# Kernel tuning notes

Hardware: AMD Instinct MI355X
Metric: run time of the kernel (lower is better)

The kernel has to match this reference:

```python
import jax, jax.numpy as jnp
import numpy as np

NUM_HEADS = 16
HEAD_DIM = 64
INPUT_DIM = 1024
EMBED_DIM = NUM_HEADS * HEAD_DIM  # 1024


def setup_inputs() -> dict:
    key = jax.random.key(0)
    ks = jax.random.split(key, 9)
    B, S = 4, 2048
    scale = 1.0 / np.sqrt(INPUT_DIM)
    return {
        "q": jax.random.normal(ks[0], (B, S, INPUT_DIM), dtype=jnp.float32),
        "k": jax.random.normal(ks[1], (B, S, INPUT_DIM), dtype=jnp.float32),
        "v": jax.random.normal(ks[2], (B, S, INPUT_DIM), dtype=jnp.float32),
        "Wq": jax.random.normal(ks[3], (INPUT_DIM, EMBED_DIM), dtype=jnp.float32) * scale,
        "bq": jax.random.normal(ks[4], (EMBED_DIM,), dtype=jnp.float32) * 0.02,
        "Wk": jax.random.normal(ks[5], (INPUT_DIM, EMBED_DIM), dtype=jnp.float32) * scale,
        "bk": jax.random.normal(ks[6], (EMBED_DIM,), dtype=jnp.float32) * 0.02,
        "Wv": jax.random.normal(ks[7], (INPUT_DIM, EMBED_DIM), dtype=jnp.float32) * scale,
        "bv": jax.random.normal(ks[8], (EMBED_DIM,), dtype=jnp.float32) * 0.02,
    }


def reference(q, k, v, Wq, bq, Wk, bk, Wv, bv):
    B, Sq, _ = q.shape
    Sk = k.shape[1]
    # QKV projections (dropout_prob=0 -> identity; ReLU on value path)
    query = (q @ Wq + bq).reshape(B, Sq, NUM_HEADS, HEAD_DIM).transpose(0, 2, 1, 3)  # [B,H,Sq,D]
    key_ = (k @ Wk + bk).reshape(B, Sk, NUM_HEADS, HEAD_DIM).transpose(0, 2, 1, 3)   # [B,H,Sk,D]
    value = jax.nn.relu(v @ Wv + bv).reshape(B, Sk, NUM_HEADS, HEAD_DIM).transpose(0, 2, 1, 3)
    scores = jnp.einsum("bhqd,bhkd->bhqk", query, key_) / np.sqrt(HEAD_DIM).astype(np.float32)
    p_attn = jax.nn.softmax(scores, axis=-1)
    x = jnp.einsum("bhqk,bhkd->bhqd", p_attn, value)  # [B,H,Sq,D]
    return x.transpose(0, 2, 1, 3).reshape(B, Sq, EMBED_DIM)
```

## Files before the change

kernel.cpp:

```cpp
#include <hip/hip_runtime.h>
#include <hip/hip_bf16.h>
#include <stdint.h>

#define BB    4
#define NH    16
#define SEQ   2048
#define DH    64
#define EMB   1024
#define KD    1024
#define MROWS 8192

typedef short  short8  __attribute__((ext_vector_type(8)));
typedef float  f32x4   __attribute__((ext_vector_type(4)));
typedef float  f32x16  __attribute__((ext_vector_type(16)));

typedef const __attribute__((address_space(1))) void* gas_t;
typedef __attribute__((address_space(3))) void*       las_t;
#define GLD16(g, l) __builtin_amdgcn_global_load_lds((gas_t)(g), (las_t)(l), 16, 0, 0)

__device__ __forceinline__ unsigned short f2bf(float f) {
    unsigned u = __float_as_uint(f);
    u += 0x7fffu + ((u >> 16) & 1u);
    return (unsigned short)(u >> 16);
}
__device__ __forceinline__ unsigned packbf(float lo, float hi) {
    union { __hip_bfloat162 h; unsigned u; } cv;
    cv.h = __float22bfloat162_rn(make_float2(lo, hi));
    return cv.u;
}

__global__ __launch_bounds__(256) void wt_kernel(const float* __restrict__ Wq,
                                                 const float* __restrict__ Wk,
                                                 const float* __restrict__ Wv,
                                                 unsigned short* __restrict__ Wt) {
    __shared__ float tsh[64 * 68];
    const int p = blockIdx.z;
    const float* W = (p == 0) ? Wq : (p == 1) ? Wk : Wv;
    unsigned short* dst = Wt + (size_t)p * (KD * EMB);
    const int k0 = blockIdx.x * 64, n0 = blockIdx.y * 64;
    const int t = threadIdx.x;
    {
        const int r = t >> 2, c4 = (t & 3) * 16;
        const float* g = W + (size_t)(k0 + r) * EMB + n0 + c4;
        float* row = &tsh[r * 68 + c4];
        *(float4*)(row + 0)  = *(const float4*)(g + 0);
        *(float4*)(row + 4)  = *(const float4*)(g + 4);
        *(float4*)(row + 8)  = *(const float4*)(g + 8);
        *(float4*)(row + 12) = *(const float4*)(g + 12);
    }
    __syncthreads();
    {
        const int j = t >> 2, kp = (t & 3) * 16;
        unsigned ub[8];
#pragma unroll
        for (int ii = 0; ii < 8; ++ii)
            ub[ii] = packbf(tsh[(kp + 2 * ii) * 68 + j], tsh[(kp + 2 * ii + 1) * 68 + j]);
        unsigned short* o = dst + (size_t)(n0 + j) * KD + k0 + kp;
        *(uint4*)(o + 0) = uint4{ub[0], ub[1], ub[2], ub[3]};
        *(uint4*)(o + 8) = uint4{ub[4], ub[5], ub[6], ub[7]};
    }
}

__global__ __launch_bounds__(256) void proj_kernel(
    const float* __restrict__ qf, const float* __restrict__ kf,
    const float* __restrict__ vf, const unsigned short* __restrict__ WtBase,
    const float* __restrict__ bq, const float* __restrict__ bk, const float* __restrict__ bv,
    unsigned short* __restrict__ Qg, unsigned short* __restrict__ Kg,
    unsigned short* __restrict__ Vt)
{
    __shared__ __align__(16) unsigned short smem[17408];
    unsigned short* Ash = smem;
    unsigned short* Bsh = smem + 8192;

    const int p = blockIdx.z;
    const float* Af = (p == 0) ? qf : (p == 1) ? kf : vf;
    const unsigned short* Wp  = WtBase  + (size_t)p * (KD * EMB);
    const float* bias = (p == 0) ? bq : (p == 1) ? bk : bv;
    unsigned short* dst = (p == 0) ? Qg : (p == 1) ? Kg : Vt;

    const int row0 = blockIdx.x * 128;
    const int col0 = blockIdx.y * 128;
    const int t = threadIdx.x, lane = t & 63, wv = t >> 6;
    const int ln15 = lane & 15, q4 = lane >> 4;
    const int wm = wv & 1, wn = wv >> 1;

    f32x4 acc[4][4];
#pragma unroll
    for (int i = 0; i < 4; ++i)
#pragma unroll
        for (int j = 0; j < 4; ++j)
#pragma unroll
            for (int r = 0; r < 4; ++r) acc[i][j][r] = 0.f;

    const int lr = lane >> 3, lc = (lane & 7) ^ lr;
    const float*          gAf = Af + (size_t)(row0 + wv * 32 + lr) * KD + lc * 8;
    const unsigned short* gB  = Wp + (size_t)(col0 + wv * 32 + lr) * KD + lc * 8;
    unsigned short* lA = Ash + wv * 32 * 64;
    unsigned short* lB = Bsh + wv * 32 * 64;

    float4 aN[4][2];
#pragma unroll
    for (int i = 0; i < 4; ++i) {
        aN[i][0] = *(const float4*)(gAf + (size_t)i * 8 * KD + 0);
        aN[i][1] = *(const float4*)(gAf + (size_t)i * 8 * KD + 4);
    }

    for (int k0 = 0; k0 < KD; k0 += 64) {
#pragma unroll
        for (int i = 0; i < 4; ++i)
            GLD16(gB + (size_t)i * 8 * KD + k0, lB + i * 512);
#pragma unroll
        for (int i = 0; i < 4; ++i) {
            uint4 u;
            u.x = packbf(aN[i][0].x, aN[i][0].y); u.y = packbf(aN[i][0].z, aN[i][0].w);
            u.z = packbf(aN[i][1].x, aN[i][1].y); u.w = packbf(aN[i][1].z, aN[i][1].w);
            *(uint4*)&lA[i * 512 + lane * 8] = u;
        }
        __syncthreads();

        if (k0 < KD - 64) {
#pragma unroll
            for (int i = 0; i < 4; ++i) {
                aN[i][0] = *(const float4*)(gAf + (size_t)i * 8 * KD + k0 + 64);
                aN[i][1] = *(const float4*)(gAf + (size_t)i * 8 * KD + k0 + 68);
            }
        }

#pragma unroll
        for (int kk = 0; kk < 2; ++kk) {
            short8 af[4], bfr[4];
#pragma unroll
            for (int mi = 0; mi < 4; ++mi) {
                const int r = wm * 64 + mi * 16 + ln15;
                af[mi] = *(const short8*)&Ash[r * 64 + (((kk << 2) | q4) ^ (r & 7)) * 8];
            }
#pragma unroll
            for (int ni = 0; ni < 4; ++ni) {
                const int r = wn * 64 + ni * 16 + ln15;
                bfr[ni] = *(const short8*)&Bsh[r * 64 + (((kk << 2) | q4) ^ (r & 7)) * 8];
            }
#pragma unroll
            for (int mi = 0; mi < 4; ++mi)
#pragma unroll
                for (int ni = 0; ni < 4; ++ni)
                    acc[mi][ni] = __builtin_amdgcn_mfma_f32_16x16x32_bf16(
                        af[mi], bfr[ni], acc[mi][ni], 0, 0, 0);
        }
        __syncthreads();
    }

    float bvv[4];
#pragma unroll
    for (int ni = 0; ni < 4; ++ni) bvv[ni] = bias[col0 + wn * 64 + ni * 16 + ln15];
    const float scq = 0.18033688011112042f;

    unsigned short* Tsh = smem;
#pragma unroll
    for (int mi = 0; mi < 4; ++mi)
#pragma unroll
        for (int ni = 0; ni < 4; ++ni)
#pragma unroll
            for (int r = 0; r < 4; ++r) {
                const int mr = wm * 64 + mi * 16 + q4 * 4 + r;
                const int ec = wn * 64 + ni * 16 + ln15;
                float vv = acc[mi][ni][r] + bvv[ni];
                if (p == 0) vv *= scq;
                if (p == 2) vv = vv > 0.f ? vv : 0.f;
                Tsh[mr * 136 + ec] = f2bf(vv);
            }
    __syncthreads();

    if (p < 2) {
        const int mr = t >> 1, hsel = t & 1;
        const int m = row0 + mr, bi = m >> 11, s = m & 2047;
        const int hh = (col0 >> 6) + hsel;
        const unsigned short* src = &Tsh[mr * 136 + hsel * 64];
        unsigned short* o = dst + ((size_t)(bi * NH + hh) * SEQ + s) * DH;
#pragma unroll
        for (int c = 0; c < 8; ++c)
            *(uint4*)(o + 8 * c) = *(const uint4*)(src + 8 * c);
    } else {
        const int e = t >> 1, sh2 = t & 1;
        const int n = col0 + e, hh = n >> 6, dd = n & 63;
        const int bi = row0 >> 11, sbase = (row0 & 2047) + sh2 * 64;
        unsigned ub[32];
#pragma unroll
        for (int i = 0; i < 32; ++i)
            ub[i] = (unsigned)Tsh[(sh2 * 64 + 2 * i) * 136 + e] |
                    ((unsigned)Tsh[(sh2 * 64 + 2 * i + 1) * 136 + e] << 16);
        unsigned short* o = dst + ((size_t)(bi * NH + hh) * DH + dd) * SEQ + sbase;
#pragma unroll
        for (int c = 0; c < 8; ++c)
            *(uint4*)(o + 8 * c) = uint4{ub[4 * c], ub[4 * c + 1], ub[4 * c + 2], ub[4 * c + 3]};
    }
}

__global__ __launch_bounds__(512) void attn_kernel(
    const unsigned short* __restrict__ Qg, const unsigned short* __restrict__ Kg,
    const unsigned short* __restrict__ Vt, float* __restrict__ out)
{
    __shared__ __align__(16) unsigned short smem[18432];

    const int lin = blockIdx.x + (blockIdx.y << 3) + (blockIdx.z << 7);
    const int g_xcd = lin & 7, s_lin = lin >> 3;
    const int qb = s_lin & 7;
    const int bh_idx = g_xcd + ((s_lin >> 3) << 3);
    const int hh = bh_idx & 15, bb = bh_idx >> 4;

    const int t = threadIdx.x, lane = t & 63, wv = t >> 6;
    const int ln31 = lane & 31, h2 = lane >> 5;
    const size_t bh = (size_t)(bb * NH + hh);
    const unsigned short* Qp = Qg + bh * (SEQ * DH);
    const unsigned short* Kp = Kg + bh * (SEQ * DH);
    const unsigned short* Vp = Vt + bh * (DH * SEQ);
    const int q0 = qb * 256 + wv * 32;

    short8 qf[4];
#pragma unroll
    for (int dc = 0; dc < 4; ++dc)
        qf[dc] = *(const short8*)(Qp + (size_t)(q0 + ln31) * DH + h2 * 8 + dc * 16);

    short8 ones;
#pragma unroll
    for (int i = 0; i < 8; ++i) ones[i] = (short)0x3F80;

    f32x16 accO[2], accL;
#pragma unroll
    for (int i = 0; i < 16; ++i) { accO[0][i] = 0.f; accO[1][i] = 0.f; accL[i] = 0.f; }

    const int srow = t >> 3, sp = (t & 7) * 8;
    const int prow = srow ^ (((((srow >> 2) ^ (srow >> 3)) & 1)) ? 12 : 0);
    const unsigned short* gk = Kp + (size_t)srow * DH + sp;
    const unsigned short* gv = Vp + (size_t)srow * SEQ + sp;
    const int wkoff = prow * 72 + sp;
    const int wvoff = 4608 + srow * 72 + sp;

    {
        short8 ka = *(const short8*)(gk);
        short8 va = *(const short8*)(gv);
        *(short8*)&smem[wkoff] = ka;
        *(short8*)&smem[wvoff] = va;
    }

    for (int it = 0; it < 32; ++it) {
        const int nxt = (it + 1) & 31;
        short8 ka = *(const short8*)(gk + (size_t)nxt * 64 * DH);
        short8 va = *(const short8*)(gv + nxt * 64);

        __syncthreads();

        const unsigned short* Ksh = smem + (it & 1) * 9216;
        const unsigned short* Vsh = Ksh + 4608;

        f32x16 st[2];
#pragma unroll
        for (int kt = 0; kt < 2; ++kt) {
#pragma unroll
            for (int i = 0; i < 16; ++i) st[kt][i] = 0.f;
#pragma unroll
            for (int dc = 0; dc < 4; ++dc) {
                short8 kf = *(const short8*)&Ksh[(kt * 32 + ln31) * 72 + h2 * 8 + dc * 16];
                st[kt] = __builtin_amdgcn_mfma_f32_32x32x16_bf16(kf, qf[dc], st[kt], 0, 0, 0);
            }
        }
#pragma unroll
        for (int kt = 0; kt < 2; ++kt)
#pragma unroll
            for (int r = 0; r < 16; ++r)
                st[kt][r] = __builtin_amdgcn_exp2f(st[kt][r]);

#pragma unroll
        for (int kt = 0; kt < 2; ++kt)
#pragma unroll
            for (int kc = 0; kc < 2; ++kc) {
                union { unsigned u[4]; short8 v; } pf;
#pragma unroll
                for (int i = 0; i < 4; ++i)
                    pf.u[i] = packbf(st[kt][8 * kc + 2 * i], st[kt][8 * kc + 2 * i + 1]);
                accL = __builtin_amdgcn_mfma_f32_32x32x16_bf16(ones, pf.v, accL, 0, 0, 0);
#pragma unroll
                for (int dt = 0; dt < 2; ++dt) {
                    short8 vf = *(const short8*)&Vsh[(dt * 32 + ln31) * 72 + kt * 32 + kc * 16 + h2 * 8];
                    accO[dt] = __builtin_amdgcn_mfma_f32_32x32x16_bf16(vf, pf.v, accO[dt], 0, 0, 0);
                }
            }

        unsigned short* wbuf = smem + ((it + 1) & 1) * 9216;
        *(short8*)&wbuf[wkoff] = ka;
        *(short8*)&wbuf[wvoff] = va;
    }

    const float inv = 1.0f / accL[0];
    float* orow = out + ((size_t)(bb * SEQ + q0 + ln31) * NH + hh) * 64;
#pragma unroll
    for (int dt = 0; dt < 2; ++dt)
#pragma unroll
        for (int g = 0; g < 4; ++g) {
            float4 w;
            w.x = accO[dt][4 * g + 0] * inv;
            w.y = accO[dt][4 * g + 1] * inv;
            w.z = accO[dt][4 * g + 2] * inv;
            w.w = accO[dt][4 * g + 3] * inv;
            *(float4*)(orow + dt * 32 + 4 * h2 + 8 * g) = w;
        }
}

extern "C" void kernel_launch(void* const* d_in, const int* in_sizes, int n_in,
                              void* d_out, int out_size, void* d_ws, size_t ws_size,
                              hipStream_t stream) {
    const float* qf = (const float*)d_in[0];
    const float* kf = (const float*)d_in[1];
    const float* vf = (const float*)d_in[2];
    const float* Wq = (const float*)d_in[3];
    const float* bq = (const float*)d_in[4];
    const float* Wk = (const float*)d_in[5];
    const float* bk = (const float*)d_in[6];
    const float* Wv = (const float*)d_in[7];
    const float* bv = (const float*)d_in[8];

    char* ws = (char*)d_ws;
    unsigned short* Wt  = (unsigned short*)ws;
    unsigned short* Qg  = (unsigned short*)(ws + 6291456);
    unsigned short* Kg  = Qg + 8388608;
    unsigned short* Vt  = Kg + 8388608;
    float* out = (float*)d_out;

    wt_kernel<<<dim3(16, 16, 3), 256, 0, stream>>>(Wq, Wk, Wv, Wt);
    proj_kernel<<<dim3(64, 8, 3), 256, 0, stream>>>(qf, kf, vf, Wt, bq, bk, bv, Qg, Kg, Vt);
    attn_kernel<<<dim3(8, 16, 4), 512, 0, stream>>>(Qg, Kg, Vt, out);
}
```

Before: 314.1 us.

## Double-buffer LDS tiles in projection GEMM to overlap loads with MFMA

The projection kernel now keeps two LDS buffers for the A and B tiles. While the current tile is consumed by MFMAs, the next B tile is issued via global_load_lds into the other buffer, and the next A tile is converted to bf16 and stored into it. This removes one barrier per k-step and hides global-to-LDS latency behind compute. In exchange it doubles shared memory to 64KB per block, which may reduce occupancy.

```diff
diff --git a/kernel.cpp b/kernel.cpp
--- a/kernel.cpp
+++ b/kernel.cpp
@@ -68,9 +68,7 @@
     unsigned short* __restrict__ Qg, unsigned short* __restrict__ Kg,
     unsigned short* __restrict__ Vt)
 {
-    __shared__ __align__(16) unsigned short smem[17408];
-    unsigned short* Ash = smem;
-    unsigned short* Bsh = smem + 8192;
+    __shared__ __align__(16) unsigned short smem[32768];
 
     const int p = blockIdx.z;
     const float* Af = (p == 0) ? qf : (p == 1) ? kf : vf;
@@ -95,34 +93,39 @@
     const int lr = lane >> 3, lc = (lane & 7) ^ lr;
     const float*          gAf = Af + (size_t)(row0 + wv * 32 + lr) * KD + lc * 8;
     const unsigned short* gB  = Wp + (size_t)(col0 + wv * 32 + lr) * KD + lc * 8;
-    unsigned short* lA = Ash + wv * 32 * 64;
-    unsigned short* lB = Bsh + wv * 32 * 64;
+    const int lAoff = wv * 2048 + lane * 8;
+    const int lBoff = 8192 + wv * 2048;
 
     float4 aN[4][2];
-#pragma unroll
-    for (int i = 0; i < 4; ++i) {
-        aN[i][0] = *(const float4*)(gAf + (size_t)i * 8 * KD + 0);
-        aN[i][1] = *(const float4*)(gAf + (size_t)i * 8 * KD + 4);
-    }
-
-    for (int k0 = 0; k0 < KD; k0 += 64) {
+
+    {
 #pragma unroll
         for (int i = 0; i < 4; ++i)
-            GLD16(gB + (size_t)i * 8 * KD + k0, lB + i * 512);
+            GLD16(gB + (size_t)i * 8 * KD, smem + lBoff + i * 512);
 #pragma unroll
         for (int i = 0; i < 4; ++i) {
+            float4 a0 = *(const float4*)(gAf + (size_t)i * 8 * KD);
+            float4 a1 = *(const float4*)(gAf + (size_t)i * 8 * KD + 4);
             uint4 u;
-            u.x = packbf(aN[i][0].x, aN[i][0].y); u.y = packbf(aN[i][0].z, aN[i][0].w);
-            u.z = packbf(aN[i][1].x, aN[i][1].y); u.w = packbf(aN[i][1].z, aN[i][1].w);
-            *(uint4*)&lA[i * 512 + lane * 8] = u;
+            u.x = packbf(a0.x, a0.y); u.y = packbf(a0.z, a0.w);
+            u.z = packbf(a1.x, a1.y); u.w = packbf(a1.z, a1.w);
+            *(uint4*)&smem[lAoff + i * 512] = u;
         }
         __syncthreads();
-
-        if (k0 < KD - 64) {
+    }
+
+    for (int k0 = 0; k0 < 16; ++k0) {
+        unsigned short* cbuf = smem + (k0 & 1) * 16384;
+        unsigned short* nbuf = smem + ((k0 + 1) & 1) * 16384;
+
+        if (k0 < 15) {
+#pragma unroll
+            for (int i = 0; i < 4; ++i)
+                GLD16(gB + (size_t)i * 8 * KD + (k0 + 1) * 64, nbuf + lBoff + i * 512);
 #pragma unroll
             for (int i = 0; i < 4; ++i) {
-                aN[i][0] = *(const float4*)(gAf + (size_t)i * 8 * KD + k0 + 64);
-                aN[i][1] = *(const float4*)(gAf + (size_t)i * 8 * KD + k0 + 68);
+                aN[i][0] = *(const float4*)(gAf + (size_t)i * 8 * KD + (k0 + 1) * 64);
+                aN[i][1] = *(const float4*)(gAf + (size_t)i * 8 * KD + (k0 + 1) * 64 + 4);
             }
         }
 
@@ -132,12 +135,12 @@
 #pragma unroll
             for (int mi = 0; mi < 4; ++mi) {
                 const int r = wm * 64 + mi * 16 + ln15;
-                af[mi] = *(const short8*)&Ash[r * 64 + (((kk << 2) | q4) ^ (r & 7)) * 8];
+                af[mi] = *(const short8*)&cbuf[r * 64 + (((kk << 2) | q4) ^ (r & 7)) * 8];
             }
 #pragma unroll
             for (int ni = 0; ni < 4; ++ni) {
                 const int r = wn * 64 + ni * 16 + ln15;
-                bfr[ni] = *(const short8*)&Bsh[r * 64 + (((kk << 2) | q4) ^ (r & 7)) * 8];
+                bfr[ni] = *(const short8*)&cbuf[8192 + r * 64 + (((kk << 2) | q4) ^ (r & 7)) * 8];
             }
 #pragma unroll
             for (int mi = 0; mi < 4; ++mi)
@@ -145,6 +148,16 @@
                 for (int ni = 0; ni < 4; ++ni)
                     acc[mi][ni] = __builtin_amdgcn_mfma_f32_16x16x32_bf16(
                         af[mi], bfr[ni], acc[mi][ni], 0, 0, 0);
+        }
+
+        if (k0 < 15) {
+#pragma unroll
+            for (int i = 0; i < 4; ++i) {
+                uint4 u;
+                u.x = packbf(aN[i][0].x, aN[i][0].y); u.y = packbf(aN[i][0].z, aN[i][0].w);
+                u.z = packbf(aN[i][1].x, aN[i][1].y); u.w = packbf(aN[i][1].z, aN[i][1].w);
+                *(uint4*)&nbuf[lAoff + i * 512] = u;
+            }
         }
         __syncthreads();
     }
```

New measurement: 339.0 us. 1.08x slower.
